# Performance work log

Measured on AMD Instinct MI355X. Metric: run time of the kernel, lower is better.

The kernel has to match this reference:

```python
import jax, jax.numpy as jnp
import numpy as np

S = 7
STEP = 1.0 / S
LAMBDA_COORD = 5.0
LAMBDA_NOOBJ = 0.5


def setup_inputs() -> dict:
    key = jax.random.key(0)
    k1, k2, k3 = jax.random.split(key, 3)
    B = 16384
    pred = jax.random.uniform(k1, (B, S, S, 30), dtype=jnp.float32)
    target = jax.random.uniform(k2, (B, S, S, 30), dtype=jnp.float32)
    conf = (jax.random.uniform(k3, (B, S, S)) > 0.9).astype(jnp.float32)
    target = target.at[..., 4].set(conf)
    return {"pred": pred, "target": target}


def _convert_box(box):
    # box: [..., S, S, 4] in cell-relative (x, y, w, h); returns clipped corners.
    gi = jnp.arange(S, dtype=box.dtype).reshape(1, S, 1)  # first spatial axis -> x offset
    gj = jnp.arange(S, dtype=box.dtype).reshape(1, 1, S)  # second spatial axis -> y offset
    x, y, w, h = box[..., 0], box[..., 1], box[..., 2], box[..., 3]
    cx = (x + gi) * STEP
    cy = (y + gj) * STEP
    x1 = jnp.maximum(cx - w / 2, 0.0)
    y1 = jnp.maximum(cy - h / 2, 0.0)
    x2 = jnp.minimum(cx + w / 2, 1.0)
    y2 = jnp.minimum(cy + h / 2, 1.0)
    return x1, y1, x2, y2


def _iou(b1, b2):
    a, b, c, d = b1
    q, w, e, r = b2
    minx = jnp.maximum(a, q)
    miny = jnp.maximum(b, w)
    maxx = jnp.minimum(c, e)
    maxy = jnp.minimum(d, r)
    inter = (maxy - miny) * (maxx - minx)  # faithful: no clamping of negative overlaps
    union = (e - q) * (r - w) + (d - b) * (c - a) - inter
    return jnp.where(inter > 0, inter / (union + 1e-05), 0.0)


def reference(pred, target):
    B = pred.shape[0]
    tbox = _convert_box(target[..., :4])
    pbox1 = _convert_box(pred[..., 0:4])
    pbox2 = _convert_box(pred[..., 5:9])
    iou1 = _iou(tbox, pbox1)  # [B, S, S]
    iou2 = _iou(tbox, pbox2)

    sel2 = iou1 <= iou2  # original: box1 responsible only if iou1 > iou2
    conf_t = jax.lax.stop_gradient(jnp.where(sel2, iou2, iou1))  # .item() detached iou
    pxy = jnp.where(sel2[..., None], pred[..., 5:7], pred[..., 0:2])
    pwh = jnp.where(sel2[..., None], pred[..., 7:9], pred[..., 2:4])
    pconf = jnp.where(sel2, pred[..., 9], pred[..., 4])

    obj = (target[..., 4] > 0).astype(pred.dtype)  # [B, S, S]
    noobj = (target[..., 4] == 0).astype(pred.dtype)

    obj_loss = jnp.sum(obj * (pconf - conf_t) ** 2)
    xy_loss = jnp.sum(obj[..., None] * (pxy - target[..., 0:2]) ** 2)
    wh_loss = jnp.sum(obj[..., None] * (pwh - target[..., 2:4]) ** 2)
    class_loss = jnp.sum(obj[..., None] * (pred[..., 10:] - target[..., 10:]) ** 2)
    noobj_loss = jnp.sum(noobj * ((pred[..., 4] - target[..., 4]) ** 2 + (pred[..., 9] - target[..., 9]) ** 2))

    loss = obj_loss + LAMBDA_NOOBJ * noobj_loss + LAMBDA_COORD * (xy_loss + wh_loss) + class_loss
    return loss / B
```

## Files before the change

kernel.cpp:

```cpp
#include <hip/hip_runtime.h>


#define NS 7
#define NC 30
#define BLOCK 256
#define F4_PER_BLOCK (BLOCK * NC / 4)

__global__ void zero_out_kernel(float* out) { out[0] = 0.0f; }

__global__ __launch_bounds__(BLOCK) void yolo_loss_kernel(
    const float* __restrict__ pred,
    const float* __restrict__ targ,
    float* __restrict__ out,
    int n_cells, float inv_B)
{
    const float STEP = 1.0f / 7.0f;
    const float L_COORD = 5.0f;
    const float L_NOOBJ = 0.5f;

    __shared__ float4 sbuf4[F4_PER_BLOCK];
    float* sbuf = (float*)sbuf4;

    const int tid = threadIdx.x;
    const int cell = blockIdx.x * BLOCK + tid;

    const float4* pg = (const float4*)pred + (size_t)blockIdx.x * F4_PER_BLOCK;
    const float4* tg = (const float4*)targ + (size_t)blockIdx.x * F4_PER_BLOCK;

    #pragma unroll
    for (int k = 0; k < 7; ++k) sbuf4[tid + k * BLOCK] = pg[tid + k * BLOCK];
    if (tid < F4_PER_BLOCK - 7 * BLOCK) sbuf4[tid + 7 * BLOCK] = pg[tid + 7 * BLOCK];
    __syncthreads();

    float p[NC];
    {
        const float2* s2 = (const float2*)sbuf + tid * (NC / 2);
        #pragma unroll
        for (int k = 0; k < NC / 2; ++k) {
            float2 v = s2[k];
            p[2 * k] = v.x;
            p[2 * k + 1] = v.y;
        }
    }
    __syncthreads();

    #pragma unroll
    for (int k = 0; k < 7; ++k) sbuf4[tid + k * BLOCK] = tg[tid + k * BLOCK];
    if (tid < F4_PER_BLOCK - 7 * BLOCK) sbuf4[tid + 7 * BLOCK] = tg[tid + 7 * BLOCK];
    __syncthreads();

    float lsum = 0.0f;
    if (cell < n_cells) {
        int j = cell % NS;
        int i = (cell / NS) % NS;
        float gi = (float)i;
        float gj = (float)j;

        const float2* s2 = (const float2*)sbuf + tid * (NC / 2);
        float2 t01 = s2[0];
        float2 t23 = s2[1];
        float2 t45 = s2[2];
        float2 t89 = s2[4];
        float t0 = t01.x, t1 = t01.y, t2 = t23.x, t3 = t23.y;
        float t4 = t45.x, t9 = t89.y;

        float ta, tb, tc, td;
        {
            float cx = (t0 + gi) * STEP;
            float cy = (t1 + gj) * STEP;
            ta = fmaxf(cx - t2 * 0.5f, 0.0f);
            tb = fmaxf(cy - t3 * 0.5f, 0.0f);
            tc = fminf(cx + t2 * 0.5f, 1.0f);
            td = fminf(cy + t3 * 0.5f, 1.0f);
        }
        float q1, w1, e1, r1;
        {
            float cx = (p[0] + gi) * STEP;
            float cy = (p[1] + gj) * STEP;
            q1 = fmaxf(cx - p[2] * 0.5f, 0.0f);
            w1 = fmaxf(cy - p[3] * 0.5f, 0.0f);
            e1 = fminf(cx + p[2] * 0.5f, 1.0f);
            r1 = fminf(cy + p[3] * 0.5f, 1.0f);
        }
        float q2, w2, e2, r2;
        {
            float cx = (p[5] + gi) * STEP;
            float cy = (p[6] + gj) * STEP;
            q2 = fmaxf(cx - p[7] * 0.5f, 0.0f);
            w2 = fmaxf(cy - p[8] * 0.5f, 0.0f);
            e2 = fminf(cx + p[7] * 0.5f, 1.0f);
            r2 = fminf(cy + p[8] * 0.5f, 1.0f);
        }

        float tarea = (td - tb) * (tc - ta);
        float iou1, iou2;
        {
            float minx = fmaxf(ta, q1), miny = fmaxf(tb, w1);
            float maxx = fminf(tc, e1), maxy = fminf(td, r1);
            float inter = (maxy - miny) * (maxx - minx);
            float uni = (e1 - q1) * (r1 - w1) + tarea - inter;
            iou1 = (inter > 0.0f) ? inter / (uni + 1e-5f) : 0.0f;
        }
        {
            float minx = fmaxf(ta, q2), miny = fmaxf(tb, w2);
            float maxx = fminf(tc, e2), maxy = fminf(td, r2);
            float inter = (maxy - miny) * (maxx - minx);
            float uni = (e2 - q2) * (r2 - w2) + tarea - inter;
            iou2 = (inter > 0.0f) ? inter / (uni + 1e-5f) : 0.0f;
        }

        bool sel2 = (iou1 <= iou2);
        float conf_t = sel2 ? iou2 : iou1;
        float px = sel2 ? p[5] : p[0];
        float py = sel2 ? p[6] : p[1];
        float pw = sel2 ? p[7] : p[2];
        float ph = sel2 ? p[8] : p[3];
        float pconf = sel2 ? p[9] : p[4];

        float obj = (t4 > 0.0f) ? 1.0f : 0.0f;
        float noobj = (t4 == 0.0f) ? 1.0f : 0.0f;

        float dx = px - t0, dy = py - t1;
        float dw = pw - t2, dh = ph - t3;
        float coord = dx * dx + dy * dy + dw * dw + dh * dh;

        float dc = pconf - conf_t;
        float obj_loss = dc * dc;

        float cls = 0.0f;
        #pragma unroll
        for (int k = 0; k < 10; ++k) {
            float2 tv = s2[5 + k];
            float d0 = p[10 + 2 * k] - tv.x;
            float d1 = p[11 + 2 * k] - tv.y;
            cls += d0 * d0;
            cls += d1 * d1;
        }

        float d4 = p[4] - t4;
        float d9 = p[9] - t9;
        float noobj_loss = d4 * d4 + d9 * d9;

        lsum = obj * (obj_loss + L_COORD * coord + cls) + L_NOOBJ * noobj * noobj_loss;
    }

    #pragma unroll
    for (int off = 32; off > 0; off >>= 1)
        lsum += __shfl_down(lsum, off, 64);

    __shared__ float wsum[4];
    int lane = threadIdx.x & 63;
    int wid = threadIdx.x >> 6;
    if (lane == 0) wsum[wid] = lsum;
    __syncthreads();
    if (threadIdx.x == 0) {
        float s = (wsum[0] + wsum[1]) + (wsum[2] + wsum[3]);
        atomicAdd(out, s * inv_B);
    }
}

extern "C" void kernel_launch(void* const* d_in, const int* in_sizes, int n_in,
                              void* d_out, int out_size, void* d_ws, size_t ws_size,
                              hipStream_t stream) {
    const float* pred = (const float*)d_in[0];
    const float* targ = (const float*)d_in[1];
    float* out = (float*)d_out;

    const int B = 16384;
    const int n_cells = B * NS * NS;
    const float inv_B = 1.0f / (float)B;

    zero_out_kernel<<<1, 1, 0, stream>>>(out);

    const int grid = (n_cells + BLOCK - 1) / BLOCK;
    yolo_loss_kernel<<<grid, BLOCK, 0, stream>>>(pred, targ, out, n_cells, inv_B);
}
```

Baseline: 206.6 us.

## Use async global-to-LDS loads and replace atomics with two-stage reduction

Loads pred and target tiles together with direct global_load_lds 16-byte copies into one doubled shared buffer, removing the register round-trip and the extra barriers between the two staging phases. It also drops the bounds check on the assumption that the cell count divides evenly by the block size. When workspace is available, per-block partials are written and a single-block reduce kernel sums them, replacing the zero kernel plus thousands of atomics. Doubling LDS per block to 60KB may cut occupancy, and the extra reduce launch adds a little latency.

```diff
diff --git a/kernel.cpp b/kernel.cpp
--- a/kernel.cpp
+++ b/kernel.cpp
@@ -4,159 +4,187 @@
 #define NS 7
 #define NC 30
 #define BLOCK 256
-#define F4_PER_BLOCK (BLOCK * NC / 4)
+#define CHUNKS 1920
+#define TARG_OFF 7680
+#define SB_FLOATS 15360
+
+typedef const __attribute__((address_space(1))) unsigned int* gas_ptr;
+typedef __attribute__((address_space(3))) unsigned int* las_ptr;
+
+__device__ __forceinline__ void async_cp16(const float* g, float* l) {
+    __builtin_amdgcn_global_load_lds((gas_ptr)g, (las_ptr)l, 16, 0, 0);
+}
 
 __global__ void zero_out_kernel(float* out) { out[0] = 0.0f; }
 
 __global__ __launch_bounds__(BLOCK) void yolo_loss_kernel(
     const float* __restrict__ pred,
     const float* __restrict__ targ,
+    float* __restrict__ partial,
     float* __restrict__ out,
-    int n_cells, float inv_B)
+    int atomic_mode, float inv_B)
 {
     const float STEP = 1.0f / 7.0f;
     const float L_COORD = 5.0f;
     const float L_NOOBJ = 0.5f;
 
-    __shared__ float4 sbuf4[F4_PER_BLOCK];
-    float* sbuf = (float*)sbuf4;
+    __shared__ float sbuf[SB_FLOATS];
 
     const int tid = threadIdx.x;
     const int cell = blockIdx.x * BLOCK + tid;
 
-    const float4* pg = (const float4*)pred + (size_t)blockIdx.x * F4_PER_BLOCK;
-    const float4* tg = (const float4*)targ + (size_t)blockIdx.x * F4_PER_BLOCK;
-
-    #pragma unroll
-    for (int k = 0; k < 7; ++k) sbuf4[tid + k * BLOCK] = pg[tid + k * BLOCK];
-    if (tid < F4_PER_BLOCK - 7 * BLOCK) sbuf4[tid + 7 * BLOCK] = pg[tid + 7 * BLOCK];
+    const float* pg = pred + (size_t)blockIdx.x * BLOCK * NC;
+    const float* tg = targ + (size_t)blockIdx.x * BLOCK * NC;
+
+    #pragma unroll
+    for (int k = 0; k < 15; ++k) {
+        int cid = k * BLOCK + tid;
+        if (cid < CHUNKS) {
+            async_cp16(pg + (size_t)cid * 4, sbuf + cid * 4);
+        } else {
+            int c2 = cid - CHUNKS;
+            async_cp16(tg + (size_t)c2 * 4, sbuf + TARG_OFF + c2 * 4);
+        }
+    }
+    asm volatile("s_waitcnt vmcnt(0)" ::: "memory");
     __syncthreads();
 
+    int j = cell % NS;
+    int i = (cell / NS) % NS;
+    float gi = (float)i;
+    float gj = (float)j;
+
     float p[NC];
     {
-        const float2* s2 = (const float2*)sbuf + tid * (NC / 2);
+        const float2* s2 = (const float2*)(sbuf) + tid * (NC / 2);
         #pragma unroll
         for (int k = 0; k < NC / 2; ++k) {
             float2 v = s2[k];
-            p[2 * k] = v.x;
-            p[2 * k + 1] = v.y;
+            p[2 * k] = v.x; p[2 * k + 1] = v.y;
         }
     }
-    __syncthreads();
-
-    #pragma unroll
-    for (int k = 0; k < 7; ++k) sbuf4[tid + k * BLOCK] = tg[tid + k * BLOCK];
-    if (tid < F4_PER_BLOCK - 7 * BLOCK) sbuf4[tid + 7 * BLOCK] = tg[tid + 7 * BLOCK];
-    __syncthreads();
-
-    float lsum = 0.0f;
-    if (cell < n_cells) {
-        int j = cell % NS;
-        int i = (cell / NS) % NS;
-        float gi = (float)i;
-        float gj = (float)j;
-
-        const float2* s2 = (const float2*)sbuf + tid * (NC / 2);
-        float2 t01 = s2[0];
-        float2 t23 = s2[1];
-        float2 t45 = s2[2];
-        float2 t89 = s2[4];
-        float t0 = t01.x, t1 = t01.y, t2 = t23.x, t3 = t23.y;
-        float t4 = t45.x, t9 = t89.y;
-
-        float ta, tb, tc, td;
-        {
-            float cx = (t0 + gi) * STEP;
-            float cy = (t1 + gj) * STEP;
-            ta = fmaxf(cx - t2 * 0.5f, 0.0f);
-            tb = fmaxf(cy - t3 * 0.5f, 0.0f);
-            tc = fminf(cx + t2 * 0.5f, 1.0f);
-            td = fminf(cy + t3 * 0.5f, 1.0f);
-        }
-        float q1, w1, e1, r1;
-        {
-            float cx = (p[0] + gi) * STEP;
-            float cy = (p[1] + gj) * STEP;
-            q1 = fmaxf(cx - p[2] * 0.5f, 0.0f);
-            w1 = fmaxf(cy - p[3] * 0.5f, 0.0f);
-            e1 = fminf(cx + p[2] * 0.5f, 1.0f);
-            r1 = fminf(cy + p[3] * 0.5f, 1.0f);
-        }
-        float q2, w2, e2, r2;
-        {
-            float cx = (p[5] + gi) * STEP;
-            float cy = (p[6] + gj) * STEP;
-            q2 = fmaxf(cx - p[7] * 0.5f, 0.0f);
-            w2 = fmaxf(cy - p[8] * 0.5f, 0.0f);
-            e2 = fminf(cx + p[7] * 0.5f, 1.0f);
-            r2 = fminf(cy + p[8] * 0.5f, 1.0f);
-        }
-
-        float tarea = (td - tb) * (tc - ta);
-        float iou1, iou2;
-        {
-            float minx = fmaxf(ta, q1), miny = fmaxf(tb, w1);
-            float maxx = fminf(tc, e1), maxy = fminf(td, r1);
-            float inter = (maxy - miny) * (maxx - minx);
-            float uni = (e1 - q1) * (r1 - w1) + tarea - inter;
-            iou1 = (inter > 0.0f) ? inter / (uni + 1e-5f) : 0.0f;
-        }
-        {
-            float minx = fmaxf(ta, q2), miny = fmaxf(tb, w2);
-            float maxx = fminf(tc, e2), maxy = fminf(td, r2);
-            float inter = (maxy - miny) * (maxx - minx);
-            float uni = (e2 - q2) * (r2 - w2) + tarea - inter;
-            iou2 = (inter > 0.0f) ? inter / (uni + 1e-5f) : 0.0f;
-        }
-
-        bool sel2 = (iou1 <= iou2);
-        float conf_t = sel2 ? iou2 : iou1;
-        float px = sel2 ? p[5] : p[0];
-        float py = sel2 ? p[6] : p[1];
-        float pw = sel2 ? p[7] : p[2];
-        float ph = sel2 ? p[8] : p[3];
-        float pconf = sel2 ? p[9] : p[4];
-
-        float obj = (t4 > 0.0f) ? 1.0f : 0.0f;
-        float noobj = (t4 == 0.0f) ? 1.0f : 0.0f;
-
-        float dx = px - t0, dy = py - t1;
-        float dw = pw - t2, dh = ph - t3;
-        float coord = dx * dx + dy * dy + dw * dw + dh * dh;
-
-        float dc = pconf - conf_t;
-        float obj_loss = dc * dc;
-
-        float cls = 0.0f;
-        #pragma unroll
-        for (int k = 0; k < 10; ++k) {
-            float2 tv = s2[5 + k];
-            float d0 = p[10 + 2 * k] - tv.x;
-            float d1 = p[11 + 2 * k] - tv.y;
-            cls += d0 * d0;
-            cls += d1 * d1;
-        }
-
-        float d4 = p[4] - t4;
-        float d9 = p[9] - t9;
-        float noobj_loss = d4 * d4 + d9 * d9;
-
-        lsum = obj * (obj_loss + L_COORD * coord + cls) + L_NOOBJ * noobj * noobj_loss;
-    }
+    const float2* s2t = (const float2*)(sbuf + TARG_OFF) + tid * (NC / 2);
+    float2 t01 = s2t[0];
+    float2 t23 = s2t[1];
+    float2 t45 = s2t[2];
+    float2 t89 = s2t[4];
+    float t0 = t01.x, t1 = t01.y, t2 = t23.x, t3 = t23.y;
+    float t4 = t45.x, t9 = t89.y;
+
+    float ta, tb, tc, td;
+    {
+        float cx = (t0 + gi) * STEP;
+        float cy = (t1 + gj) * STEP;
+        ta = fmaxf(cx - t2 * 0.5f, 0.0f);
+        tb = fmaxf(cy - t3 * 0.5f, 0.0f);
+        tc = fminf(cx + t2 * 0.5f, 1.0f);
+        td = fminf(cy + t3 * 0.5f, 1.0f);
+    }
+    float q1, w1, e1, r1;
+    {
+        float cx = (p[0] + gi) * STEP;
+        float cy = (p[1] + gj) * STEP;
+        q1 = fmaxf(cx - p[2] * 0.5f, 0.0f);
+        w1 = fmaxf(cy - p[3] * 0.5f, 0.0f);
+        e1 = fminf(cx + p[2] * 0.5f, 1.0f);
+        r1 = fminf(cy + p[3] * 0.5f, 1.0f);
+    }
+    float q2, w2, e2, r2;
+    {
+        float cx = (p[5] + gi) * STEP;
+        float cy = (p[6] + gj) * STEP;
+        q2 = fmaxf(cx - p[7] * 0.5f, 0.0f);
+        w2 = fmaxf(cy - p[8] * 0.5f, 0.0f);
+        e2 = fminf(cx + p[7] * 0.5f, 1.0f);
+        r2 = fminf(cy + p[8] * 0.5f, 1.0f);
+    }
+
+    float tarea = (td - tb) * (tc - ta);
+    float iou1, iou2;
+    {
+        float minx = fmaxf(ta, q1), miny = fmaxf(tb, w1);
+        float maxx = fminf(tc, e1), maxy = fminf(td, r1);
+        float inter = (maxy - miny) * (maxx - minx);
+        float uni = (e1 - q1) * (r1 - w1) + tarea - inter;
+        iou1 = (inter > 0.0f) ? inter / (uni + 1e-5f) : 0.0f;
+    }
+    {
+        float minx = fmaxf(ta, q2), miny = fmaxf(tb, w2);
+        float maxx = fminf(tc, e2), maxy = fminf(td, r2);
+        float inter = (maxy - miny) * (maxx - minx);
+        float uni = (e2 - q2) * (r2 - w2) + tarea - inter;
+        iou2 = (inter > 0.0f) ? inter / (uni + 1e-5f) : 0.0f;
+    }
+
+    bool sel2 = (iou1 <= iou2);
+    float conf_t = sel2 ? iou2 : iou1;
+    float px = sel2 ? p[5] : p[0];
+    float py = sel2 ? p[6] : p[1];
+    float pw = sel2 ? p[7] : p[2];
+    float ph = sel2 ? p[8] : p[3];
+    float pconf = sel2 ? p[9] : p[4];
+
+    float obj = (t4 > 0.0f) ? 1.0f : 0.0f;
+    float noobj = (t4 == 0.0f) ? 1.0f : 0.0f;
+
+    float dx = px - t0, dy = py - t1;
+    float dw = pw - t2, dh = ph - t3;
+    float coord = dx * dx + dy * dy + dw * dw + dh * dh;
+
+    float dc = pconf - conf_t;
+    float obj_loss = dc * dc;
+
+    float cls = 0.0f;
+    #pragma unroll
+    for (int k = 0; k < 10; ++k) {
+        float2 tv = s2t[5 + k];
+        float d0 = p[10 + 2 * k] - tv.x;
+        float d1 = p[11 + 2 * k] - tv.y;
+        cls += d0 * d0;
+        cls += d1 * d1;
+    }
+
+    float d4 = p[4] - t4;
+    float d9 = p[9] - t9;
+    float noobj_loss = d4 * d4 + d9 * d9;
+
+    float lsum = obj * (obj_loss + L_COORD * coord + cls) + L_NOOBJ * noobj * noobj_loss;
 
     #pragma unroll
     for (int off = 32; off > 0; off >>= 1)
         lsum += __shfl_down(lsum, off, 64);
 
     __shared__ float wsum[4];
-    int lane = threadIdx.x & 63;
-    int wid = threadIdx.x >> 6;
+    int lane = tid & 63;
+    int wid = tid >> 6;
     if (lane == 0) wsum[wid] = lsum;
     __syncthreads();
-    if (threadIdx.x == 0) {
+    if (tid == 0) {
         float s = (wsum[0] + wsum[1]) + (wsum[2] + wsum[3]);
-        atomicAdd(out, s * inv_B);
-    }
+        if (atomic_mode) atomicAdd(out, s * inv_B);
+        else partial[blockIdx.x] = s;
+    }
+}
+
+__global__ __launch_bounds__(BLOCK) void reduce_kernel(
+    const float* __restrict__ partial, float* __restrict__ out,
+    int n, float inv_B)
+{
+    const int tid = threadIdx.x;
+    float s = 0.0f;
+    for (int idx = tid; idx < n; idx += BLOCK) s += partial[idx];
+
+    #pragma unroll
+    for (int off = 32; off > 0; off >>= 1)
+        s += __shfl_down(s, off, 64);
+
+    __shared__ float wsum[4];
+    int lane = tid & 63;
+    int wid = tid >> 6;
+    if (lane == 0) wsum[wid] = s;
+    __syncthreads();
+    if (tid == 0)
+        out[0] = ((wsum[0] + wsum[1]) + (wsum[2] + wsum[3])) * inv_B;
 }
 
 extern "C" void kernel_launch(void* const* d_in, const int* in_sizes, int n_in,
@@ -169,9 +197,14 @@
     const int B = 16384;
     const int n_cells = B * NS * NS;
     const float inv_B = 1.0f / (float)B;
-
-    zero_out_kernel<<<1, 1, 0, stream>>>(out);
-
-    const int grid = (n_cells + BLOCK - 1) / BLOCK;
-    yolo_loss_kernel<<<grid, BLOCK, 0, stream>>>(pred, targ, out, n_cells, inv_B);
-}
+    const int grid = n_cells / BLOCK;
+
+    if (ws_size >= (size_t)grid * sizeof(float) && d_ws != nullptr) {
+        float* partial = (float*)d_ws;
+        yolo_loss_kernel<<<grid, BLOCK, 0, stream>>>(pred, targ, partial, out, 0, inv_B);
+        reduce_kernel<<<1, BLOCK, 0, stream>>>(partial, out, grid, inv_B);
+    } else {
+        zero_out_kernel<<<1, 1, 0, stream>>>(out);
+        yolo_loss_kernel<<<grid, BLOCK, 0, stream>>>(pred, targ, nullptr, out, 1, inv_B);
+    }
+}
```

New measurement: 206.1 us. About the same (-0.3%).
